# Kernel optimization log

Hardware: AMD Instinct MI355X
Metric: run time of the kernel (lower is better)

## Reference

```python
import jax, jax.numpy as jnp
import numpy as np

B, S, D, H = 4, 1024, 1024, 16
HD = D // H


def setup_inputs() -> dict:
    key = jax.random.key(0)
    ks = jax.random.split(key, 8)
    x = jax.random.normal(ks[0], (B, S, D), dtype=jnp.float32)
    attn_bias = jax.random.normal(ks[1], (B, H, S, S), dtype=jnp.float32) * 0.1
    pos_ids = jnp.broadcast_to(jnp.arange(S, dtype=jnp.int32), (B, S))
    lengths = jnp.array([S, S - 64, S - 128, S - 256], dtype=jnp.int32)
    pad_mask = jnp.arange(S)[None, :] >= lengths[:, None]  # True = padded key
    scale = 0.02
    Wq = jax.random.normal(ks[2], (D, D), dtype=jnp.float32) * scale
    Wk = jax.random.normal(ks[3], (D, D), dtype=jnp.float32) * scale
    Wv = jax.random.normal(ks[4], (D, D), dtype=jnp.float32) * scale
    Wo = jax.random.normal(ks[5], (D, D), dtype=jnp.float32) * scale
    bq = jnp.zeros((D,), jnp.float32); bk = jnp.zeros((D,), jnp.float32)
    bv = jnp.zeros((D,), jnp.float32); bo = jnp.zeros((D,), jnp.float32)
    return {"x": x, "attn_bias": attn_bias, "pos_ids": pos_ids, "pad_mask": pad_mask,
            "Wq": Wq, "bq": bq, "Wk": Wk, "bk": bk, "Wv": Wv, "bv": bv, "Wo": Wo, "bo": bo}


def _apply_rotary(q, k, pos_ids):
    # q,k: [B,S,H,HD]; pos_ids: [B,S]
    hd = q.shape[-1]
    inv_freq = 1.0 / (10000.0 ** (jnp.arange(0, hd, 2, dtype=jnp.float32) / hd))
    freqs = pos_ids.astype(jnp.float32)[:, :, None] * inv_freq  # [B,S,HD/2]
    emb = jnp.concatenate([freqs, freqs], axis=-1)[:, :, None, :]  # [B,S,1,HD]
    cos, sin = jnp.cos(emb), jnp.sin(emb)
    def rot_half(t):
        t1, t2 = jnp.split(t, 2, axis=-1)
        return jnp.concatenate([-t2, t1], axis=-1)
    return q * cos + rot_half(q) * sin, k * cos + rot_half(k) * sin


def reference(x, attn_bias, pos_ids, pad_mask, Wq, bq, Wk, bk, Wv, bv, Wo, bo):
    b, s, d = x.shape
    q = (x @ Wq.T + bq).reshape(b, s, H, HD)
    k = (x @ Wk.T + bk).reshape(b, s, H, HD)
    v = (x @ Wv.T + bv).reshape(b, s, H, HD)
    q, k = _apply_rotary(q, k, pos_ids)
    q = q.transpose(0, 2, 1, 3)  # [B,H,S,HD]
    k = k.transpose(0, 2, 1, 3)
    v = v.transpose(0, 2, 1, 3)
    scores = jnp.einsum("bhqd,bhkd->bhqk", q, k) / np.sqrt(HD).astype(np.float32)
    scores = scores + attn_bias
    scores = jnp.where(pad_mask[:, None, None, :], -jnp.inf, scores)
    attn = jax.nn.softmax(scores, axis=-1)  # dropout p=0 -> identity
    out = jnp.einsum("bhqk,bhkd->bqhd", attn, v).reshape(b, s, d)
    metric = k.mean(axis=1)  # mean over heads -> [B,S,HD]
    return out @ Wo.T + bo, metric
```

## Files before the change

kernel.cpp:

```cpp
#include <hip/hip_runtime.h>
#include <hip/hip_bf16.h>

#define SS 1024
#define DD 1024
#define HH 16
#define HDD 64

using f32x4  = __attribute__((ext_vector_type(4))) float;
using bf16x8 = __attribute__((ext_vector_type(8))) __bf16;
using bf16x4 = __attribute__((ext_vector_type(4))) __bf16;

__device__ __forceinline__ void gload_lds16(const void* g, void* l) {
  __builtin_amdgcn_global_load_lds((__attribute__((address_space(1))) void*)g,
                                   (__attribute__((address_space(3))) void*)l, 16, 0, 0);
}

__global__ void convert_kernel(const float4* __restrict__ x, const float4* __restrict__ Wq,
                               const float4* __restrict__ Wk, const float4* __restrict__ Wv,
                               const float4* __restrict__ Wo,
                               bf16x4* __restrict__ xb, bf16x4* __restrict__ wqkvb,
                               bf16x4* __restrict__ wob, float4* __restrict__ metric) {
  int i = blockIdx.x * 256 + threadIdx.x;
  if (blockIdx.x < 256) {
    float4 z = {0.f, 0.f, 0.f, 0.f};
    metric[blockIdx.x * 256 + threadIdx.x] = z;
  }
  float4 v; bf16x4* dst;
  if (i < 1048576)      { v = x[i];              dst = xb + i; }
  else if (i < 1310720) { v = Wq[i - 1048576];   dst = wqkvb + (i - 1048576); }
  else if (i < 1572864) { v = Wk[i - 1310720];   dst = wqkvb + 262144 + (i - 1310720); }
  else if (i < 1835008) { v = Wv[i - 1572864];   dst = wqkvb + 524288 + (i - 1572864); }
  else                  { v = Wo[i - 1835008];   dst = wob + (i - 1835008); }
  bf16x4 o;
  o[0] = (__bf16)v.x; o[1] = (__bf16)v.y; o[2] = (__bf16)v.z; o[3] = (__bf16)v.w;
  *dst = o;
}

#define GEMM_STAGE(BUF, KK)                                                        \
  {                                                                                \
    char* Ab = smem + (BUF) * 32768;                                               \
    char* Bb = Ab + 16384;                                                         \
    _Pragma("unroll") for (int q = 0; q < 4; ++q) {                                \
      int idx = q * 256 + tid;                                                     \
      int row = idx >> 3, c = idx & 7;                                             \
      gload_lds16(A  + (size_t)(m0 + row) * 1024 + (KK) + ((c ^ (row & 7)) << 3),  \
                  Ab + q * 4096 + wid * 1024);                                     \
      gload_lds16(Bm + (size_t)(n0 + row) * 1024 + (KK) + ((c ^ (row & 7)) << 3),  \
                  Bb + q * 4096 + wid * 1024);                                     \
    }                                                                              \
  }

template<int EPI>
__global__ __launch_bounds__(256, 2)
void gemm_kernel(const __bf16* __restrict__ A, const __bf16* __restrict__ Bm, int N,
                 const float* __restrict__ b0, const float* __restrict__ b1,
                 const float* __restrict__ b2, const int* __restrict__ pos_ids,
                 __bf16* __restrict__ Qr, __bf16* __restrict__ Kr, __bf16* __restrict__ Vtg,
                 float* __restrict__ metric, float* __restrict__ Cout) {
  __shared__ __align__(16) char smem[65536];
  const int tid = threadIdx.x;
  const int wid = tid >> 6, lane = tid & 63;
  const int g = lane >> 4, cl = lane & 15;
  const int ntn = N >> 7;
  const int tile = (blockIdx.x & 7) * ((int)gridDim.x >> 3) + (blockIdx.x >> 3);
  const int bm = tile / ntn, bn = tile % ntn;
  const int m0 = bm << 7, n0 = bn << 7;
  const int wr = (wid >> 1) << 6, wc = (wid & 1) << 6;
  const int swz = cl & 7;

  f32x4 acc[4][4] = {};

  GEMM_STAGE(0, 0);
  __syncthreads();
  int buf = 0;
  for (int t = 0; t < 16; ++t) {
    if (t + 1 < 16) GEMM_STAGE(buf ^ 1, (t + 1) * 64);
    const __bf16* Abuf = (const __bf16*)(smem + buf * 32768);
    const __bf16* Bbuf = Abuf + 8192;
#pragma unroll
    for (int s = 0; s < 2; ++s) {
      bf16x8 fa[4], fb[4];
#pragma unroll
      for (int i = 0; i < 4; ++i)
        fa[i] = *(const bf16x8*)(Abuf + (wr + i * 16 + cl) * 64 + (((s * 4 + g) ^ swz) << 3));
#pragma unroll
      for (int j = 0; j < 4; ++j)
        fb[j] = *(const bf16x8*)(Bbuf + (wc + j * 16 + cl) * 64 + (((s * 4 + g) ^ swz) << 3));
#pragma unroll
      for (int i = 0; i < 4; ++i)
#pragma unroll
        for (int j = 0; j < 4; ++j)
          acc[i][j] = __builtin_amdgcn_mfma_f32_16x16x32_bf16(fa[i], fb[j], acc[i][j], 0, 0, 0);
    }
    __syncthreads();
    buf ^= 1;
  }

  if constexpr (EPI == 1) {
#pragma unroll
    for (int j = 0; j < 4; ++j) {
      int col = n0 + wc + j * 16 + cl;
      float bv = b0[col];
#pragma unroll
      for (int i = 0; i < 4; ++i)
#pragma unroll
        for (int r = 0; r < 4; ++r) {
          int row = m0 + wr + i * 16 + g * 4 + r;
          Cout[(size_t)row * 1024 + col] = acc[i][j][r] + bv;
        }
    }
  } else if (n0 >= 2048) {
    __bf16* vt_s = (__bf16*)smem;
    const int b_ = m0 >> 10, s0 = m0 & 1023;
    const int vbase = n0 - 2048;
#pragma unroll
    for (int phase = 0; phase < 2; ++phase) {
      __syncthreads();
      if ((wid & 1) == phase) {
#pragma unroll
        for (int j = 0; j < 4; ++j) {
          int d = j * 16 + cl;
          float bv = b2[vbase + wc + d];
#pragma unroll
          for (int i = 0; i < 4; ++i)
#pragma unroll
            for (int r = 0; r < 4; ++r)
              vt_s[d * 136 + wr + i * 16 + g * 4 + r] = (__bf16)(acc[i][j][r] + bv);
        }
      }
      __syncthreads();
      int hh = (vbase >> 6) + phase;
#pragma unroll
      for (int p = 0; p < 4; ++p) {
        int d = p * 16 + (tid >> 4), s8 = (tid & 15) * 8;
        bf16x8 v = *(const bf16x8*)(vt_s + d * 136 + s8);
        *(bf16x8*)(Vtg + ((size_t)(b_ * HH + hh) * HDD + d) * SS + s0 + s8) = v;
      }
    }
  } else {
    const int cb = n0 + wc;
    const int region = cb >> 10;
    const int hcol = (cb & 1023) >> 6;
    const int cir = cb & 1023;
    const float* bias = region == 0 ? b0 : b1;
    __bf16* dst = region == 0 ? Qr : Kr;
    float invf0 = exp2f(-0.4152410118609203f * (float)(cl));
    float invf1 = exp2f(-0.4152410118609203f * (float)(16 + cl));
#pragma unroll
    for (int i = 0; i < 4; ++i) {
#pragma unroll
      for (int r = 0; r < 4; ++r) {
        int row = m0 + wr + i * 16 + g * 4 + r;
        int b_ = row >> 10, s = row & 1023;
        size_t ob = ((size_t)(b_ * HH + hcol) * SS + s) * HDD;
        float pos = (float)pos_ids[row];
#pragma unroll
        for (int j = 0; j < 2; ++j) {
          int dlo = j * 16 + cl;
          float vlo = acc[i][j][r]     + bias[cir + dlo];
          float vhi = acc[i][j + 2][r] + bias[cir + dlo + 32];
          float th = pos * (j == 0 ? invf0 : invf1);
          float sn, cs;
          __sincosf(th, &sn, &cs);
          float olo = vlo * cs - vhi * sn;
          float ohi = vhi * cs + vlo * sn;
          dst[ob + dlo]      = (__bf16)olo;
          dst[ob + dlo + 32] = (__bf16)ohi;
          if (region == 1) {
            atomicAdd(&metric[(size_t)row * HDD + dlo],      olo * 0.0625f);
            atomicAdd(&metric[(size_t)row * HDD + dlo + 32], ohi * 0.0625f);
          }
        }
      }
    }
  }
}

#define TILE_BODY(T, BUF, BCUR, BNXT)                                              \
  {                                                                                \
    __syncthreads();                                                               \
    if ((T) + 1 < ntile) {                                                         \
      const int kk = ((T) + 1) * 64;                                               \
      gload_lds16(Kb + (size_t)(kk + krow) * 64 + kchk * 8,                        \
                  (char*)&Ks[(BUF) ^ 1][8 * wid][0]);                              \
      gload_lds16(Vb + (size_t)krow * SS + kk + kchk * 8,                          \
                  (char*)&Vt[(BUF) ^ 1][8 * wid][0]);                              \
      _Pragma("unroll") for (int kt = 0; kt < 4; ++kt)                             \
        _Pragma("unroll") for (int r = 0; r < 4; ++r)                              \
          BNXT[kt][r] = Bb[(size_t)(q0 + 4 * g + r) * SS + kk + kt * 16 + cl];     \
    }                                                                              \
    f32x4 sc[4];                                                                   \
    __builtin_amdgcn_s_setprio(1);                                                 \
    _Pragma("unroll") for (int kt = 0; kt < 4; ++kt) {                             \
      bf16x8 kb0 = *(const bf16x8*)(&Ks[(BUF)][kt * 16 + cl][(g ^ swz) * 8]);      \
      bf16x8 kb1 = *(const bf16x8*)(&Ks[(BUF)][kt * 16 + cl][((g + 4) ^ swz) * 8]);\
      f32x4 z = {0.f, 0.f, 0.f, 0.f};                                              \
      z = __builtin_amdgcn_mfma_f32_16x16x32_bf16(aq0, kb0, z, 0, 0, 0);           \
      sc[kt] = __builtin_amdgcn_mfma_f32_16x16x32_bf16(aq1, kb1, z, 0, 0, 0);      \
    }                                                                              \
    __builtin_amdgcn_s_setprio(0);                                                 \
    _Pragma("unroll") for (int kt = 0; kt < 4; ++kt)                               \
      _Pragma("unroll") for (int r = 0; r < 4; ++r)                                \
        sc[kt][r] = sc[kt][r] * 0.125f + BCUR[kt][r];                              \
    float mx[4];                                                                   \
    _Pragma("unroll") for (int r = 0; r < 4; ++r)                                  \
      mx[r] = fmaxf(fmaxf(sc[0][r], sc[1][r]), fmaxf(sc[2][r], sc[3][r]));         \
    _Pragma("unroll") for (int d = 1; d < 16; d <<= 1)                             \
      _Pragma("unroll") for (int r = 0; r < 4; ++r)                                \
        mx[r] = fmaxf(mx[r], __shfl_xor(mx[r], d, 64));                            \
    bool adv = true;                                                               \
    _Pragma("unroll") for (int r = 0; r < 4; ++r)                                  \
      adv = adv && (mx[r] <= m_l[r] + 8.0f);                                       \
    if (!__all(adv)) {                                                             \
      _Pragma("unroll") for (int r = 0; r < 4; ++r) {                              \
        float nm = fmaxf(m_l[r], mx[r]);                                           \
        float s_ = __expf(m_l[r] - nm);                                            \
        m_l[r] = nm; l_l[r] *= s_;                                                 \
        _Pragma("unroll") for (int dj = 0; dj < 4; ++dj) o[dj][r] *= s_;           \
      }                                                                            \
    }                                                                              \
    _Pragma("unroll") for (int kt = 0; kt < 4; ++kt)                               \
      _Pragma("unroll") for (int r = 0; r < 4; ++r)                                \
        sc[kt][r] = __expf(sc[kt][r] - m_l[r]);                                    \
    _Pragma("unroll") for (int kt = 0; kt < 4; ++kt)                               \
      _Pragma("unroll") for (int r = 0; r < 4; ++r)                                \
        Plds[wid][g * 4 + r][kt * 16 + cl] = (__bf16)sc[kt][r];                    \
    bf16x8 pa0 = *(const bf16x8*)(&Plds[wid][cl][g * 8]);                          \
    bf16x8 pa1 = *(const bf16x8*)(&Plds[wid][cl][32 + g * 8]);                     \
    __builtin_amdgcn_s_setprio(1);                                                 \
    f32x4 ls = {0.f, 0.f, 0.f, 0.f};                                               \
    ls = __builtin_amdgcn_mfma_f32_16x16x32_bf16(pa0, onesb, ls, 0, 0, 0);         \
    ls = __builtin_amdgcn_mfma_f32_16x16x32_bf16(pa1, onesb, ls, 0, 0, 0);         \
    _Pragma("unroll") for (int dj = 0; dj < 4; ++dj) {                             \
      bf16x8 vb0 = *(const bf16x8*)(&Vt[(BUF)][dj * 16 + cl][(g ^ swz) * 8]);      \
      bf16x8 vb1 = *(const bf16x8*)(&Vt[(BUF)][dj * 16 + cl][((g + 4) ^ swz) * 8]);\
      o[dj] = __builtin_amdgcn_mfma_f32_16x16x32_bf16(pa0, vb0, o[dj], 0, 0, 0);   \
      o[dj] = __builtin_amdgcn_mfma_f32_16x16x32_bf16(pa1, vb1, o[dj], 0, 0, 0);   \
    }                                                                              \
    __builtin_amdgcn_s_setprio(0);                                                 \
    _Pragma("unroll") for (int r = 0; r < 4; ++r) l_l[r] += ls[r];                 \
  }

__global__ __launch_bounds__(512, 4)
void attn_kernel(const __bf16* __restrict__ Qr, const __bf16* __restrict__ Kr,
                 const __bf16* __restrict__ Vtg, const float* __restrict__ bias,
                 const int* __restrict__ pad, __bf16* __restrict__ attn_out) {
  __shared__ __align__(16) __bf16 Ks[2][64][64];
  __shared__ __align__(16) __bf16 Vt[2][64][64];
  __shared__ __align__(16) __bf16 Plds[8][16][68];
  const int tid = threadIdx.x;
  const int wid = tid >> 6, lane = tid & 63;
  const int g = lane >> 4, cl = lane & 15;
  const int bh = blockIdx.x & 63, b_ = bh >> 4, h = bh & 15;
  const int q0 = (blockIdx.x >> 6) * 128 + wid * 16;
  const __bf16* Qb = Qr  + ((size_t)bh << 16);
  const __bf16* Kb = Kr  + ((size_t)bh << 16);
  const __bf16* Vb = Vtg + ((size_t)bh << 16);
  const float*  Bb = bias + ((size_t)bh << 20);
  const int* padb = pad + b_ * SS;

  int pm = (lane < 16) ? padb[lane * 64] : 1;
  unsigned long long ball = __ballot(pm == 0);
  const int ntile = __popcll(ball & 0xFFFFull);

  const int l8 = lane >> 3, l7 = lane & 7;
  const int krow = 8 * wid + l8;
  const int kchk = l7 ^ l8;
  const int swz = cl & 7;

  gload_lds16(Kb + (size_t)krow * 64 + kchk * 8, (char*)&Ks[0][8 * wid][0]);
  gload_lds16(Vb + (size_t)krow * SS + kchk * 8, (char*)&Vt[0][8 * wid][0]);
  float bregA[4][4], bregB[4][4];
#pragma unroll
  for (int kt = 0; kt < 4; ++kt)
#pragma unroll
    for (int r = 0; r < 4; ++r)
      bregA[kt][r] = Bb[(size_t)(q0 + 4 * g + r) * SS + kt * 16 + cl];

  bf16x8 aq0 = *(const bf16x8*)(Qb + (size_t)(q0 + cl) * 64 + g * 8);
  bf16x8 aq1 = *(const bf16x8*)(Qb + (size_t)(q0 + cl) * 64 + 32 + g * 8);
  bf16x8 onesb;
#pragma unroll
  for (int j = 0; j < 8; ++j) onesb[j] = (__bf16)1.0f;

  f32x4 o[4] = {};
  float m_l[4] = {-1e30f, -1e30f, -1e30f, -1e30f};
  float l_l[4] = {0.f, 0.f, 0.f, 0.f};

  for (int t = 0; t < ntile; t += 2) {
    TILE_BODY(t, 0, bregA, bregB);
    if (t + 1 < ntile) TILE_BODY(t + 1, 1, bregB, bregA);
  }

#pragma unroll
  for (int dj = 0; dj < 4; ++dj)
#pragma unroll
    for (int r = 0; r < 4; ++r) {
      int qrow = q0 + g * 4 + r;
      attn_out[(size_t)(b_ * SS + qrow) * DD + h * 64 + dj * 16 + cl] =
          (__bf16)(o[dj][r] / l_l[r]);
    }
}

extern "C" void kernel_launch(void* const* d_in, const int* in_sizes, int n_in,
                              void* d_out, int out_size, void* d_ws, size_t ws_size,
                              hipStream_t stream) {
  const float* x  = (const float*)d_in[0];
  const float* ab = (const float*)d_in[1];
  const int* pos  = (const int*)d_in[2];
  const int* pad  = (const int*)d_in[3];
  const float* Wq = (const float*)d_in[4];
  const float* bq = (const float*)d_in[5];
  const float* Wk = (const float*)d_in[6];
  const float* bk = (const float*)d_in[7];
  const float* Wv = (const float*)d_in[8];
  const float* bv = (const float*)d_in[9];
  const float* Wo = (const float*)d_in[10];
  const float* bo = (const float*)d_in[11];
  float* out = (float*)d_out;
  float* metric = out + 4194304;

  char* ws = (char*)d_ws;
  __bf16* Qr   = (__bf16*)(ws);
  __bf16* Kr   = (__bf16*)(ws + 8388608);
  __bf16* Vtg  = (__bf16*)(ws + 16777216);
  __bf16* xb   = (__bf16*)(ws + 25165824);
  __bf16* wqkv = (__bf16*)(ws + 33554432);
  __bf16* wob  = (__bf16*)(ws + 39845888);
  __bf16* ao   = (__bf16*)(ws + 41943040);

  convert_kernel<<<8192, 256, 0, stream>>>((const float4*)x, (const float4*)Wq,
                                           (const float4*)Wk, (const float4*)Wv,
                                           (const float4*)Wo, (bf16x4*)xb,
                                           (bf16x4*)wqkv, (bf16x4*)wob, (float4*)metric);
  gemm_kernel<0><<<768, 256, 0, stream>>>(xb, wqkv, 3072, bq, bk, bv, pos,
                                          Qr, Kr, Vtg, metric, nullptr);
  attn_kernel<<<512, 512, 0, stream>>>(Qr, Kr, Vtg, ab, pad, ao);
  gemm_kernel<1><<<256, 256, 0, stream>>>(ao, wob, 1024, bo, nullptr, nullptr, nullptr,
                                          nullptr, nullptr, nullptr, nullptr, out);
}
```

Measured before the change: 161.1 us.

## Transpose QK^T MFMA so each lane owns one query row in attention

Swaps the MFMA operand order for the score computation, so the score tile comes out transposed and each lane holds scores for a single query row. Row max and row sum then need only two cross-lane shuffles, softmax state becomes scalar per lane, and the ones-vector MFMA for the row sum is dropped. The bias is now loaded as contiguous float4 vectors, and P is written to LDS as packed bf16x4 with a padded stride of 72. In exchange, rescale factors and final normalizers must be shuffled back into the output-accumulator layout, which adds some cross-lane traffic.

```diff
diff --git a/kernel.cpp b/kernel.cpp
--- a/kernel.cpp
+++ b/kernel.cpp
@@ -178,7 +178,7 @@
 
 #define TILE_BODY(T, BUF, BCUR, BNXT)                                              \
   {                                                                                \
-    __syncthreads();                                                               \
+    __syncthreads();                        \
     if ((T) + 1 < ntile) {                                                         \
       const int kk = ((T) + 1) * 64;                                               \
       gload_lds16(Kb + (size_t)(kk + krow) * 64 + kchk * 8,                        \
@@ -186,8 +186,7 @@
       gload_lds16(Vb + (size_t)krow * SS + kk + kchk * 8,                          \
                   (char*)&Vt[(BUF) ^ 1][8 * wid][0]);                              \
       _Pragma("unroll") for (int kt = 0; kt < 4; ++kt)                             \
-        _Pragma("unroll") for (int r = 0; r < 4; ++r)                              \
-          BNXT[kt][r] = Bb[(size_t)(q0 + 4 * g + r) * SS + kk + kt * 16 + cl];     \
+        BNXT[kt] = *(const f32x4*)(Bb + (size_t)(q0 + cl) * SS + kk + kt * 16 + 4 * g); \
     }                                                                              \
     f32x4 sc[4];                                                                   \
     __builtin_amdgcn_s_setprio(1);                                                 \
@@ -195,42 +194,48 @@
       bf16x8 kb0 = *(const bf16x8*)(&Ks[(BUF)][kt * 16 + cl][(g ^ swz) * 8]);      \
       bf16x8 kb1 = *(const bf16x8*)(&Ks[(BUF)][kt * 16 + cl][((g + 4) ^ swz) * 8]);\
       f32x4 z = {0.f, 0.f, 0.f, 0.f};                                              \
-      z = __builtin_amdgcn_mfma_f32_16x16x32_bf16(aq0, kb0, z, 0, 0, 0);           \
-      sc[kt] = __builtin_amdgcn_mfma_f32_16x16x32_bf16(aq1, kb1, z, 0, 0, 0);      \
+      z = __builtin_amdgcn_mfma_f32_16x16x32_bf16(kb0, aq0, z, 0, 0, 0);           \
+      sc[kt] = __builtin_amdgcn_mfma_f32_16x16x32_bf16(kb1, aq1, z, 0, 0, 0);      \
     }                                                                              \
     __builtin_amdgcn_s_setprio(0);                                                 \
     _Pragma("unroll") for (int kt = 0; kt < 4; ++kt)                               \
       _Pragma("unroll") for (int r = 0; r < 4; ++r)                                \
         sc[kt][r] = sc[kt][r] * 0.125f + BCUR[kt][r];                              \
-    float mx[4];                                                                   \
-    _Pragma("unroll") for (int r = 0; r < 4; ++r)                                  \
-      mx[r] = fmaxf(fmaxf(sc[0][r], sc[1][r]), fmaxf(sc[2][r], sc[3][r]));         \
-    _Pragma("unroll") for (int d = 1; d < 16; d <<= 1)                             \
-      _Pragma("unroll") for (int r = 0; r < 4; ++r)                                \
-        mx[r] = fmaxf(mx[r], __shfl_xor(mx[r], d, 64));                            \
-    bool adv = true;                                                               \
-    _Pragma("unroll") for (int r = 0; r < 4; ++r)                                  \
-      adv = adv && (mx[r] <= m_l[r] + 8.0f);                                       \
-    if (!__all(adv)) {                                                             \
-      _Pragma("unroll") for (int r = 0; r < 4; ++r) {                              \
-        float nm = fmaxf(m_l[r], mx[r]);                                           \
-        float s_ = __expf(m_l[r] - nm);                                            \
-        m_l[r] = nm; l_l[r] *= s_;                                                 \
-        _Pragma("unroll") for (int dj = 0; dj < 4; ++dj) o[dj][r] *= s_;           \
+    float mx = fmaxf(fmaxf(fmaxf(sc[0][0], sc[0][1]), fmaxf(sc[0][2], sc[0][3])),  \
+                     fmaxf(fmaxf(sc[1][0], sc[1][1]), fmaxf(sc[1][2], sc[1][3]))); \
+    mx = fmaxf(mx, fmaxf(fmaxf(fmaxf(sc[2][0], sc[2][1]), fmaxf(sc[2][2], sc[2][3])), \
+                         fmaxf(fmaxf(sc[3][0], sc[3][1]), fmaxf(sc[3][2], sc[3][3])))); \
+    mx = fmaxf(mx, __shfl_xor(mx, 16, 64));                                        \
+    mx = fmaxf(mx, __shfl_xor(mx, 32, 64));                                        \
+    if (!__all(mx <= m_l + 8.0f)) {                                                \
+      float nm = fmaxf(m_l, mx);                                                   \
+      float s_ = __expf(m_l - nm);                                                 \
+      m_l = nm; l_l *= s_;                                                         \
+      float sb0 = __shfl(s_, 4 * g + 0, 64), sb1 = __shfl(s_, 4 * g + 1, 64);      \
+      float sb2 = __shfl(s_, 4 * g + 2, 64), sb3 = __shfl(s_, 4 * g + 3, 64);      \
+      _Pragma("unroll") for (int dj = 0; dj < 4; ++dj) {                           \
+        o[dj][0] *= sb0; o[dj][1] *= sb1; o[dj][2] *= sb2; o[dj][3] *= sb3;        \
       }                                                                            \
     }                                                                              \
     _Pragma("unroll") for (int kt = 0; kt < 4; ++kt)                               \
       _Pragma("unroll") for (int r = 0; r < 4; ++r)                                \
-        sc[kt][r] = __expf(sc[kt][r] - m_l[r]);                                    \
-    _Pragma("unroll") for (int kt = 0; kt < 4; ++kt)                               \
-      _Pragma("unroll") for (int r = 0; r < 4; ++r)                                \
-        Plds[wid][g * 4 + r][kt * 16 + cl] = (__bf16)sc[kt][r];                    \
+        sc[kt][r] = __expf(sc[kt][r] - m_l);                                       \
+    float rs = ((sc[0][0] + sc[0][1]) + (sc[0][2] + sc[0][3]))                     \
+             + ((sc[1][0] + sc[1][1]) + (sc[1][2] + sc[1][3]))                     \
+             + ((sc[2][0] + sc[2][1]) + (sc[2][2] + sc[2][3]))                     \
+             + ((sc[3][0] + sc[3][1]) + (sc[3][2] + sc[3][3]));                    \
+    rs += __shfl_xor(rs, 16, 64);                                                  \
+    rs += __shfl_xor(rs, 32, 64);                                                  \
+    l_l += rs;                                                                     \
+    _Pragma("unroll") for (int kt = 0; kt < 4; ++kt) {                             \
+      bf16x4 pk;                                                                   \
+      pk[0] = (__bf16)sc[kt][0]; pk[1] = (__bf16)sc[kt][1];                        \
+      pk[2] = (__bf16)sc[kt][2]; pk[3] = (__bf16)sc[kt][3];                        \
+      *(bf16x4*)(&Plds[wid][cl][kt * 16 + 4 * g]) = pk;                            \
+    }                                                                              \
     bf16x8 pa0 = *(const bf16x8*)(&Plds[wid][cl][g * 8]);                          \
     bf16x8 pa1 = *(const bf16x8*)(&Plds[wid][cl][32 + g * 8]);                     \
     __builtin_amdgcn_s_setprio(1);                                                 \
-    f32x4 ls = {0.f, 0.f, 0.f, 0.f};                                               \
-    ls = __builtin_amdgcn_mfma_f32_16x16x32_bf16(pa0, onesb, ls, 0, 0, 0);         \
-    ls = __builtin_amdgcn_mfma_f32_16x16x32_bf16(pa1, onesb, ls, 0, 0, 0);         \
     _Pragma("unroll") for (int dj = 0; dj < 4; ++dj) {                             \
       bf16x8 vb0 = *(const bf16x8*)(&Vt[(BUF)][dj * 16 + cl][(g ^ swz) * 8]);      \
       bf16x8 vb1 = *(const bf16x8*)(&Vt[(BUF)][dj * 16 + cl][((g + 4) ^ swz) * 8]);\
@@ -238,7 +243,6 @@
       o[dj] = __builtin_amdgcn_mfma_f32_16x16x32_bf16(pa1, vb1, o[dj], 0, 0, 0);   \
     }                                                                              \
     __builtin_amdgcn_s_setprio(0);                                                 \
-    _Pragma("unroll") for (int r = 0; r < 4; ++r) l_l[r] += ls[r];                 \
   }
 
 __global__ __launch_bounds__(512, 4)
@@ -247,7 +251,7 @@
                  const int* __restrict__ pad, __bf16* __restrict__ attn_out) {
   __shared__ __align__(16) __bf16 Ks[2][64][64];
   __shared__ __align__(16) __bf16 Vt[2][64][64];
-  __shared__ __align__(16) __bf16 Plds[8][16][68];
+  __shared__ __align__(16) __bf16 Plds[8][16][72];
   const int tid = threadIdx.x;
   const int wid = tid >> 6, lane = tid & 63;
   const int g = lane >> 4, cl = lane & 15;
@@ -268,38 +272,35 @@
   const int kchk = l7 ^ l8;
   const int swz = cl & 7;
 
+  bf16x8 aq0 = *(const bf16x8*)(Qb + (size_t)(q0 + cl) * 64 + g * 8);
+  bf16x8 aq1 = *(const bf16x8*)(Qb + (size_t)(q0 + cl) * 64 + 32 + g * 8);
+
   gload_lds16(Kb + (size_t)krow * 64 + kchk * 8, (char*)&Ks[0][8 * wid][0]);
   gload_lds16(Vb + (size_t)krow * SS + kchk * 8, (char*)&Vt[0][8 * wid][0]);
-  float bregA[4][4], bregB[4][4];
+  f32x4 bregA[4], bregB[4];
 #pragma unroll
   for (int kt = 0; kt < 4; ++kt)
-#pragma unroll
-    for (int r = 0; r < 4; ++r)
-      bregA[kt][r] = Bb[(size_t)(q0 + 4 * g + r) * SS + kt * 16 + cl];
-
-  bf16x8 aq0 = *(const bf16x8*)(Qb + (size_t)(q0 + cl) * 64 + g * 8);
-  bf16x8 aq1 = *(const bf16x8*)(Qb + (size_t)(q0 + cl) * 64 + 32 + g * 8);
-  bf16x8 onesb;
-#pragma unroll
-  for (int j = 0; j < 8; ++j) onesb[j] = (__bf16)1.0f;
+    bregA[kt] = *(const f32x4*)(Bb + (size_t)(q0 + cl) * SS + kt * 16 + 4 * g);
 
   f32x4 o[4] = {};
-  float m_l[4] = {-1e30f, -1e30f, -1e30f, -1e30f};
-  float l_l[4] = {0.f, 0.f, 0.f, 0.f};
+  float m_l = -1e30f, l_l = 0.f;
 
   for (int t = 0; t < ntile; t += 2) {
     TILE_BODY(t, 0, bregA, bregB);
     if (t + 1 < ntile) TILE_BODY(t + 1, 1, bregB, bregA);
   }
 
-#pragma unroll
-  for (int dj = 0; dj < 4; ++dj)
-#pragma unroll
-    for (int r = 0; r < 4; ++r) {
-      int qrow = q0 + g * 4 + r;
-      attn_out[(size_t)(b_ * SS + qrow) * DD + h * 64 + dj * 16 + cl] =
-          (__bf16)(o[dj][r] / l_l[r]);
-    }
+  float lb0 = __shfl(l_l, 4 * g + 0, 64), lb1 = __shfl(l_l, 4 * g + 1, 64);
+  float lb2 = __shfl(l_l, 4 * g + 2, 64), lb3 = __shfl(l_l, 4 * g + 3, 64);
+  float ib0 = 1.f / lb0, ib1 = 1.f / lb1, ib2 = 1.f / lb2, ib3 = 1.f / lb3;
+#pragma unroll
+  for (int dj = 0; dj < 4; ++dj) {
+    int col = h * 64 + dj * 16 + cl;
+    attn_out[(size_t)(b_ * SS + q0 + g * 4 + 0) * DD + col] = (__bf16)(o[dj][0] * ib0);
+    attn_out[(size_t)(b_ * SS + q0 + g * 4 + 1) * DD + col] = (__bf16)(o[dj][1] * ib1);
+    attn_out[(size_t)(b_ * SS + q0 + g * 4 + 2) * DD + col] = (__bf16)(o[dj][2] * ib2);
+    attn_out[(size_t)(b_ * SS + q0 + g * 4 + 3) * DD + col] = (__bf16)(o[dj][3] * ib3);
+  }
 }
 
 extern "C" void kernel_launch(void* const* d_in, const int* in_sizes, int n_in,
```

New measurement: 158.7 us. No clear change (-1.5%).
